# Performance work log

Measured on AMD Instinct MI355X. Metric: run time of the kernel, lower is better.

The kernel has to match this reference:

```python
import jax, jax.numpy as jnp
import numpy as np

N_NODES = 100000
N_EDGES = 3200000
N_FEAT = 128
HIDDEN = 16
N_CLASSES = 10
N_GRAPHS = 64


def gcn_conv(x, W, b, src, dst, num_nodes):
    # PyG GCNConv: h = x W; add self-loops; norm = deg^{-1/2}[src]*deg^{-1/2}[dst]
    h = x @ W  # [N, out]
    deg = jax.ops.segment_sum(jnp.ones(src.shape[0], h.dtype), dst,
                              num_segments=num_nodes) + 1.0  # self-loop
    dinv = jax.lax.rsqrt(deg)
    coef = dinv[src] * dinv[dst]  # [E]
    agg = jax.ops.segment_sum(h[src] * coef[:, None], dst,
                              num_segments=num_nodes)
    # self-loop contribution: norm = dinv[i]^2
    agg = agg + h * (dinv * dinv)[:, None]
    return agg + b


def setup_inputs() -> dict:
    key = jax.random.key(0)
    k1, k2, k3, k4, k5, k6, k7 = jax.random.split(key, 7)
    x = jax.random.normal(k1, (N_NODES, N_FEAT), dtype=jnp.float32)
    edge_index = jax.random.randint(k2, (2, N_EDGES), 0, N_NODES, dtype=jnp.int64)
    batch = jnp.sort(jax.random.randint(k3, (N_NODES,), 0, N_GRAPHS, dtype=jnp.int64))
    W1 = jax.random.normal(k4, (N_FEAT, HIDDEN), dtype=jnp.float32) / np.sqrt(N_FEAT)
    b1 = jnp.zeros((HIDDEN,), jnp.float32)
    W2 = jax.random.normal(k5, (HIDDEN, N_CLASSES), dtype=jnp.float32) / np.sqrt(HIDDEN)
    b2 = jnp.zeros((N_CLASSES,), jnp.float32)
    return {"x": x, "edge_index": edge_index, "batch": batch,
            "W1": W1, "b1": b1, "W2": W2, "b2": b2}


def reference(x, edge_index, batch, W1, b1, W2, b2):
    src, dst = edge_index[0], edge_index[1]
    h = gcn_conv(x, W1, b1, src, dst, N_NODES)
    h = jax.nn.relu(h)
    h = gcn_conv(h, W2, b2, src, dst, N_NODES)  # [N, C]
    # global mean pool per graph
    sums = jax.ops.segment_sum(h, batch, num_segments=N_GRAPHS)
    cnts = jax.ops.segment_sum(jnp.ones(N_NODES, h.dtype), batch,
                               num_segments=N_GRAPHS)
    pooled = sums / jnp.maximum(cnts, 1.0)[:, None]  # [G, C]
    return jax.nn.log_softmax(pooled, axis=1)
```

## Files before the change

kernel.cpp:

```cpp
#include <hip/hip_runtime.h>
#include <hip/hip_fp16.h>

#define N_NODES   100000
#define N_EDGES   3200000
#define N_FEAT    128
#define HIDDEN    16
#define N_CLASSES 10
#define N_GRAPHS  64

#define NBUCK     391
#define CAP       9216
#define BINA_EPB  16384
#define BINA_BLOCKS ((N_EDGES + BINA_EPB - 1) / BINA_EPB)


__global__ __launch_bounds__(512) void k_ginit(int* __restrict__ gcur,
                                               float* __restrict__ pooled) {
    int t = threadIdx.x;
    if (t < NBUCK) gcur[t] = t * CAP;
    pooled[t] = 0.f;
    pooled[t + 512] = 0.f;
}

__global__ __launch_bounds__(1024) void k_binA(const int* __restrict__ src,
                                               const int* __restrict__ dst,
                                               int* __restrict__ gcur,
                                               int* __restrict__ stage) {
    __shared__ int hist[NBUCK];
    __shared__ int curb[NBUCK];
    int tid = threadIdx.x;
    long long base = (long long)blockIdx.x * BINA_EPB;
    for (int t = tid; t < NBUCK; t += 1024) hist[t] = 0;
    __syncthreads();
    int se[16], de[16];
#pragma unroll
    for (int i = 0; i < 16; ++i) {
        long long e = base + i * 1024 + tid;
        if (e < N_EDGES) {
            se[i] = src[e];
            de[i] = dst[e];
            atomicAdd(&hist[de[i] >> 8], 1);
        } else {
            de[i] = -1;
        }
    }
    __syncthreads();
    for (int t = tid; t < NBUCK; t += 1024) {
        int h = hist[t];
        curb[t] = h ? atomicAdd(&gcur[t], h) : 0;
    }
    __syncthreads();
#pragma unroll
    for (int i = 0; i < 16; ++i) {
        if (de[i] >= 0) {
            int b = de[i] >> 8;
            int p = atomicAdd(&curb[b], 1);
            stage[p] = (se[i] << 8) | (de[i] & 255);
        }
    }
}

__global__ __launch_bounds__(512) void k_binB(const int* __restrict__ gcur,
                                              const int* __restrict__ stage,
                                              int2* __restrict__ be,
                                              float* __restrict__ dinv,
                                              int* __restrict__ srcs) {
    __shared__ int hist[256];
    __shared__ int excl[256];
    int b = blockIdx.x, tid = threadIdx.x;
    int cnt   = gcur[b] - b * CAP;
    int sbase = b * CAP;
    if (tid < 256) hist[tid] = 0;
    __syncthreads();
    int nvec = cnt >> 2;
    for (int i = tid; i < nvec; i += 512) {
        int4 v = *(const int4*)&stage[sbase + i * 4];
        atomicAdd(&hist[v.x & 255], 1);
        atomicAdd(&hist[v.y & 255], 1);
        atomicAdd(&hist[v.z & 255], 1);
        atomicAdd(&hist[v.w & 255], 1);
    }
    if (tid < (cnt & 3)) {
        int v = stage[sbase + (nvec << 2) + tid];
        atomicAdd(&hist[v & 255], 1);
    }
    __syncthreads();
    int c = 0, ex = 0;
    if (tid < 256) {
        c = hist[tid];
        excl[tid] = c;
    }
    __syncthreads();
    for (int o = 1; o < 256; o <<= 1) {
        int a = 0;
        if (tid < 256 && tid >= o) a = excl[tid - o];
        __syncthreads();
        if (tid < 256) excl[tid] += a;
        __syncthreads();
    }
    if (tid < 256) {
        ex = excl[tid] - c;
        int node = b * 256 + tid;
        if (node < N_NODES) {
            be[node]   = make_int2(sbase + ex, sbase + ex + c);
            dinv[node] = rsqrtf((float)c + 1.0f);
        }
    }
    __syncthreads();
    if (tid < 256) hist[tid] = ex;
    __syncthreads();
    for (int i = tid; i < nvec; i += 512) {
        int4 v = *(const int4*)&stage[sbase + i * 4];
        int p0 = atomicAdd(&hist[v.x & 255], 1);
        int p1 = atomicAdd(&hist[v.y & 255], 1);
        int p2 = atomicAdd(&hist[v.z & 255], 1);
        int p3 = atomicAdd(&hist[v.w & 255], 1);
        srcs[sbase + p0] = v.x >> 8;
        srcs[sbase + p1] = v.y >> 8;
        srcs[sbase + p2] = v.z >> 8;
        srcs[sbase + p3] = v.w >> 8;
    }
    if (tid < (cnt & 3)) {
        int v = stage[sbase + (nvec << 2) + tid];
        int p = atomicAdd(&hist[v & 255], 1);
        srcs[sbase + p] = v >> 8;
    }
}

__global__ __launch_bounds__(256) void k_gemm1(const float* __restrict__ x,
                                               const float* __restrict__ W1,
                                               const float* __restrict__ dinv,
                                               __half* __restrict__ h1h) {
    __shared__ float w[N_FEAT * HIDDEN];
    __shared__ float xs[16 * N_FEAT];
    __shared__ float ds[16];
    int tid  = threadIdx.x;
    int base = blockIdx.x * 16;
    if (tid < 16) ds[tid] = dinv[base + tid];
    const float4* w4 = (const float4*)W1;
    float4*       wd = (float4*)w;
    wd[tid]       = w4[tid];
    wd[256 + tid] = w4[256 + tid];
    const float4* x4 = (const float4*)(x + (long long)base * N_FEAT);
    float4*       xd = (float4*)xs;
    xd[tid]       = x4[tid];
    xd[256 + tid] = x4[256 + tid];
    __syncthreads();
    int n = tid >> 4, c = tid & 15;
    const float* xr = &xs[n * N_FEAT];
    float acc = 0.f;
#pragma unroll
    for (int k = 0; k < N_FEAT; ++k) acc += xr[k] * w[k * HIDDEN + c];
    h1h[(base + n) * HIDDEN + c] = __float2half(acc * ds[n]);
}

#define NT(p) __builtin_nontemporal_load(p)

#define GATHER_DEF(TBL)                                                       \
    float acc[8];                                                             \
    _Pragma("unroll") for (int q = 0; q < 8; ++q) acc[q] = 0.f;               \
    {                                                                         \
        int ne = end - beg;                                                   \
        int nr = ne >> 3;                                                     \
        int j  = beg + k;                                                     \
        int npair = nr >> 1;                                                  \
        if (npair > 0) {                                                      \
            int sA = NT(&srcs[j]), sB = NT(&srcs[j + 8]);                     \
            for (int p = 1; p < npair; ++p) {                                 \
                int sC = NT(&srcs[j + 16]), sD = NT(&srcs[j + 24]);           \
                GACC(TBL, sA); GACC(TBL, sB);                                 \
                sA = sC; sB = sD; j += 16;                                    \
            }                                                                 \
            GACC(TBL, sA); GACC(TBL, sB); j += 16;                            \
        }                                                                     \
        if (nr & 1) { int sA = NT(&srcs[j]); GACC(TBL, sA); j += 8; }         \
        if (k < (ne & 7)) { int sA = NT(&srcs[j]); GACC(TBL, sA); }           \
    }                                                                         \
    _Pragma("unroll") for (int m = 2; m <= 8; m <<= 1) {                      \
        _Pragma("unroll") for (int q = 0; q < 8; ++q)                         \
            acc[q] += __shfl_xor(acc[q], m, 64);                              \
    }

#define GACC(TBL, S) {                                                        \
    float4 g_ = *(const float4*)(&TBL[(S) * 16 + h * 8]);                     \
    const __half2* hp_ = (const __half2*)&g_;                                 \
    float2 v0_ = __half22float2(hp_[0]);                                      \
    float2 v1_ = __half22float2(hp_[1]);                                      \
    float2 v2_ = __half22float2(hp_[2]);                                      \
    float2 v3_ = __half22float2(hp_[3]);                                      \
    acc[0] += v0_.x; acc[1] += v0_.y; acc[2] += v1_.x; acc[3] += v1_.y;       \
    acc[4] += v2_.x; acc[5] += v2_.y; acc[6] += v3_.x; acc[7] += v3_.y; }

__global__ __launch_bounds__(256) void k_agg1(const int2* __restrict__ be,
                                              const int* __restrict__ srcs,
                                              const float* __restrict__ dinv,
                                              const __half* __restrict__ h1h,
                                              const float* __restrict__ b1,
                                              const float* __restrict__ W2,
                                              __half* __restrict__ h2h) {
    __shared__ float r_s[16][17];
    __shared__ float w2s[HIDDEN * N_CLASSES];
    int tid = threadIdx.x;
    if (tid < HIDDEN * N_CLASSES) w2s[tid] = W2[tid];
    int nl = tid >> 4, l = tid & 15, k = l >> 1, h = l & 1;
    int n  = blockIdx.x * 16 + nl;
    int2 bn = be[n];
    int beg = bn.x, end = bn.y;
    GATHER_DEF(h1h)
    if (l < 2) {
#pragma unroll
        for (int q = 0; q < 8; ++q) r_s[nl][h * 8 + q] = acc[q];
    }
    __syncthreads();
    float dn   = dinv[n];
    float self = __half2float(h1h[n * 16 + l]);
    float val  = fmaxf(dn * (r_s[nl][l] + self) + b1[l], 0.f);
    __syncthreads();
    r_s[nl][l] = val;
    __syncthreads();
    float o = 0.f;
    if (l < N_CLASSES) {
#pragma unroll
        for (int q = 0; q < HIDDEN; ++q) o += r_s[nl][q] * w2s[q * N_CLASSES + l];
        o *= dn;
    }
    h2h[n * 16 + l] = __float2half(o);
}

__global__ __launch_bounds__(256) void k_agg2p(const int2* __restrict__ be,
                                               const int* __restrict__ srcs,
                                               const float* __restrict__ dinv,
                                               const __half* __restrict__ h2h,
                                               const int* __restrict__ batch,
                                               float* __restrict__ pooled) {
    __shared__ float red[16][17];
    int tid = threadIdx.x;
    int nl = tid >> 4, l = tid & 15, k = l >> 1, h = l & 1;
    int nbase = blockIdx.x * 16;
    int n  = nbase + nl;
    int2 bn = be[n];
    int beg = bn.x, end = bn.y;
    GATHER_DEF(h2h)
    if (l < 2) {
#pragma unroll
        for (int q = 0; q < 8; ++q) red[nl][h * 8 + q] = acc[q];
    }
    __syncthreads();
    float self = __half2float(h2h[n * 16 + l]);
    float o = dinv[n] * (red[nl][l] + self);
    __syncthreads();

    int g0  = batch[nbase];
    int g15 = batch[nbase + 15];
    if (g0 == g15) {
        red[nl][l] = o;
        __syncthreads();
#pragma unroll
        for (int s = 8; s > 0; s >>= 1) {
            if (nl < s) red[nl][l] += red[nl + s][l];
            __syncthreads();
        }
        if (tid < N_CLASSES) atomicAdd(&pooled[g0 * 16 + tid], red[0][tid]);
    } else {
        if (l < N_CLASSES) atomicAdd(&pooled[batch[n] * 16 + l], o);
    }
}

__global__ __launch_bounds__(64) void k_final(const float* __restrict__ pooled,
                                              const float* __restrict__ b2,
                                              const int* __restrict__ batch,
                                              float* __restrict__ out) {
    int g = threadIdx.x;
    if (g >= N_GRAPHS) return;
    int lo = 0, hi = N_NODES;
    while (lo < hi) { int m = (lo + hi) >> 1; if (batch[m] < g) lo = m + 1; else hi = m; }
    int start = lo;
    lo = 0; hi = N_NODES;
    while (lo < hi) { int m = (lo + hi) >> 1; if (batch[m] < g + 1) lo = m + 1; else hi = m; }
    int cnt = lo - start;

    float v[N_CLASSES];
    if (cnt > 0) {
        float inv = 1.f / (float)cnt;
#pragma unroll
        for (int j = 0; j < N_CLASSES; ++j) v[j] = pooled[g * 16 + j] * inv + b2[j];
    } else {
#pragma unroll
        for (int j = 0; j < N_CLASSES; ++j) v[j] = 0.f;
    }
    float m = v[0];
#pragma unroll
    for (int j = 1; j < N_CLASSES; ++j) m = fmaxf(m, v[j]);
    float l = 0.f;
#pragma unroll
    for (int j = 0; j < N_CLASSES; ++j) l += expf(v[j] - m);
    l = logf(l);
#pragma unroll
    for (int j = 0; j < N_CLASSES; ++j) out[g * N_CLASSES + j] = v[j] - m - l;
}

extern "C" void kernel_launch(void* const* d_in, const int* in_sizes, int n_in,
                              void* d_out, int out_size, void* d_ws, size_t ws_size,
                              hipStream_t stream) {
    const float* x     = (const float*)d_in[0];
    const int*   edge  = (const int*)d_in[1];
    const int*   batch = (const int*)d_in[2];
    const float* W1    = (const float*)d_in[3];
    const float* b1    = (const float*)d_in[4];
    const float* W2    = (const float*)d_in[5];
    const float* b2    = (const float*)d_in[6];
    float* out = (float*)d_out;
    float* ws  = (float*)d_ws;

    int*    gcur   = (int*)ws;
    float*  pooled = ws + 512;
    float*  dinv   = ws + 1536;
    int2*   be     = (int2*)(ws + 101536);
    int*    srcs   = (int*)(ws + 301536);
    int*    stage  = (int*)(ws + 3904992);
    __half* h1h    = (__half*)(ws + 3904992);
    __half* h2h    = (__half*)(ws + 4704992);

    const int* srcp = edge;
    const int* dstp = edge + N_EDGES;

    k_ginit<<<1, 512, 0, stream>>>(gcur, pooled);
    k_binA<<<BINA_BLOCKS, 1024, 0, stream>>>(srcp, dstp, gcur, stage);
    k_binB<<<NBUCK, 512, 0, stream>>>(gcur, stage, be, dinv, srcs);
    k_gemm1<<<N_NODES / 16, 256, 0, stream>>>(x, W1, dinv, h1h);
    k_agg1<<<N_NODES / 16, 256, 0, stream>>>(be, srcs, dinv, h1h, b1, W2, h2h);
    k_agg2p<<<N_NODES / 16, 256, 0, stream>>>(be, srcs, dinv, h2h, batch, pooled);
    k_final<<<1, 64, 0, stream>>>(pooled, b2, batch, out);
}
```

Measured before the change: 238.6 us.

## Replace atomic bucket binning with per-block fixed slots and vectorize gemm1

The edge binning no longer claims space in each bucket with global atomics. Each binA block now writes its bucket counts into a per-block, per-bucket table, and its edges go into a fixed 128-entry slot for that (block, bucket) pair. binB reads those counts and walks the scattered slots with one wavefront per slot before doing the local counting sort. In gemm1, W1 is transposed into padded shared memory so the dot product uses float4 loads, and the init kernel becomes a memset. The risks are a much larger staging buffer, less contiguous reads in binB, and silent overflow if any (block, bucket) cell exceeds 128 edges.

```diff
diff --git a/kernel.cpp b/kernel.cpp
--- a/kernel.cpp
+++ b/kernel.cpp
@@ -10,21 +10,14 @@
 
 #define NBUCK     391
 #define CAP       9216
+#define SLOT      128
 #define BINA_EPB  16384
 #define BINA_BLOCKS ((N_EDGES + BINA_EPB - 1) / BINA_EPB)
 
 
-__global__ __launch_bounds__(512) void k_ginit(int* __restrict__ gcur,
-                                               float* __restrict__ pooled) {
-    int t = threadIdx.x;
-    if (t < NBUCK) gcur[t] = t * CAP;
-    pooled[t] = 0.f;
-    pooled[t + 512] = 0.f;
-}
-
 __global__ __launch_bounds__(1024) void k_binA(const int* __restrict__ src,
                                                const int* __restrict__ dst,
-                                               int* __restrict__ gcur,
+                                               int* __restrict__ gcnt,
                                                int* __restrict__ stage) {
     __shared__ int hist[NBUCK];
     __shared__ int curb[NBUCK];
@@ -45,9 +38,10 @@
         }
     }
     __syncthreads();
+    int cellbase = blockIdx.x * NBUCK;
     for (int t = tid; t < NBUCK; t += 1024) {
-        int h = hist[t];
-        curb[t] = h ? atomicAdd(&gcur[t], h) : 0;
+        gcnt[cellbase + t] = hist[t];
+        curb[t] = (cellbase + t) * SLOT;
     }
     __syncthreads();
 #pragma unroll
@@ -60,36 +54,30 @@
     }
 }
 
-__global__ __launch_bounds__(512) void k_binB(const int* __restrict__ gcur,
-                                              const int* __restrict__ stage,
-                                              int2* __restrict__ be,
-                                              float* __restrict__ dinv,
-                                              int* __restrict__ srcs) {
+__global__ __launch_bounds__(1024) void k_binB(const int* __restrict__ gcnt,
+                                               const int* __restrict__ stage,
+                                               int2* __restrict__ be,
+                                               float* __restrict__ dinv,
+                                               int* __restrict__ srcs) {
     __shared__ int hist[256];
     __shared__ int excl[256];
+    __shared__ int scnt[BINA_BLOCKS];
     int b = blockIdx.x, tid = threadIdx.x;
-    int cnt   = gcur[b] - b * CAP;
-    int sbase = b * CAP;
     if (tid < 256) hist[tid] = 0;
-    __syncthreads();
-    int nvec = cnt >> 2;
-    for (int i = tid; i < nvec; i += 512) {
-        int4 v = *(const int4*)&stage[sbase + i * 4];
-        atomicAdd(&hist[v.x & 255], 1);
-        atomicAdd(&hist[v.y & 255], 1);
-        atomicAdd(&hist[v.z & 255], 1);
-        atomicAdd(&hist[v.w & 255], 1);
-    }
-    if (tid < (cnt & 3)) {
-        int v = stage[sbase + (nvec << 2) + tid];
-        atomicAdd(&hist[v & 255], 1);
-    }
-    __syncthreads();
-    int c = 0, ex = 0;
-    if (tid < 256) {
-        c = hist[tid];
-        excl[tid] = c;
-    }
+    for (int s = tid; s < BINA_BLOCKS; s += 1024) scnt[s] = gcnt[s * NBUCK + b];
+    __syncthreads();
+    int wid = tid >> 6, lane = tid & 63;
+    for (int s = wid; s < BINA_BLOCKS; s += 16) {
+        int c  = scnt[s];
+        int sb = (s * NBUCK + b) * SLOT;
+        for (int i = lane; i < c; i += 64) {
+            int v = stage[sb + i];
+            atomicAdd(&hist[v & 255], 1);
+        }
+    }
+    __syncthreads();
+    int c = 0;
+    if (tid < 256) { c = hist[tid]; excl[tid] = c; }
     __syncthreads();
     for (int o = 1; o < 256; o <<= 1) {
         int a = 0;
@@ -98,8 +86,9 @@
         if (tid < 256) excl[tid] += a;
         __syncthreads();
     }
+    int sbase = b * CAP;
     if (tid < 256) {
-        ex = excl[tid] - c;
+        int ex = excl[tid] - c;
         int node = b * 256 + tid;
         if (node < N_NODES) {
             be[node]   = make_int2(sbase + ex, sbase + ex + c);
@@ -107,23 +96,16 @@
         }
     }
     __syncthreads();
-    if (tid < 256) hist[tid] = ex;
-    __syncthreads();
-    for (int i = tid; i < nvec; i += 512) {
-        int4 v = *(const int4*)&stage[sbase + i * 4];
-        int p0 = atomicAdd(&hist[v.x & 255], 1);
-        int p1 = atomicAdd(&hist[v.y & 255], 1);
-        int p2 = atomicAdd(&hist[v.z & 255], 1);
-        int p3 = atomicAdd(&hist[v.w & 255], 1);
-        srcs[sbase + p0] = v.x >> 8;
-        srcs[sbase + p1] = v.y >> 8;
-        srcs[sbase + p2] = v.z >> 8;
-        srcs[sbase + p3] = v.w >> 8;
-    }
-    if (tid < (cnt & 3)) {
-        int v = stage[sbase + (nvec << 2) + tid];
-        int p = atomicAdd(&hist[v & 255], 1);
-        srcs[sbase + p] = v >> 8;
+    if (tid < 256) hist[tid] = excl[tid] - c;
+    __syncthreads();
+    for (int s = wid; s < BINA_BLOCKS; s += 16) {
+        int cc = scnt[s];
+        int sb = (s * NBUCK + b) * SLOT;
+        for (int i = lane; i < cc; i += 64) {
+            int v = stage[sb + i];
+            int p = atomicAdd(&hist[v & 255], 1);
+            srcs[sbase + p] = v >> 8;
+        }
     }
 }
 
@@ -131,26 +113,36 @@
                                                const float* __restrict__ W1,
                                                const float* __restrict__ dinv,
                                                __half* __restrict__ h1h) {
-    __shared__ float w[N_FEAT * HIDDEN];
+    __shared__ float wT[16][132];
     __shared__ float xs[16 * N_FEAT];
     __shared__ float ds[16];
     int tid  = threadIdx.x;
     int base = blockIdx.x * 16;
     if (tid < 16) ds[tid] = dinv[base + tid];
     const float4* w4 = (const float4*)W1;
-    float4*       wd = (float4*)w;
-    wd[tid]       = w4[tid];
-    wd[256 + tid] = w4[256 + tid];
+    float4 wa = w4[tid], wb = w4[256 + tid];
+    {
+        int r = tid >> 2, cb = (tid & 3) * 4;
+        wT[cb + 0][r] = wa.x; wT[cb + 1][r] = wa.y;
+        wT[cb + 2][r] = wa.z; wT[cb + 3][r] = wa.w;
+        int r2 = r + 64;
+        wT[cb + 0][r2] = wb.x; wT[cb + 1][r2] = wb.y;
+        wT[cb + 2][r2] = wb.z; wT[cb + 3][r2] = wb.w;
+    }
     const float4* x4 = (const float4*)(x + (long long)base * N_FEAT);
     float4*       xd = (float4*)xs;
     xd[tid]       = x4[tid];
     xd[256 + tid] = x4[256 + tid];
     __syncthreads();
     int n = tid >> 4, c = tid & 15;
-    const float* xr = &xs[n * N_FEAT];
+    const float4* xv = (const float4*)&xs[n * N_FEAT];
+    const float4* wv = (const float4*)&wT[c][0];
     float acc = 0.f;
 #pragma unroll
-    for (int k = 0; k < N_FEAT; ++k) acc += xr[k] * w[k * HIDDEN + c];
+    for (int k4 = 0; k4 < 32; ++k4) {
+        float4 a = xv[k4], w = wv[k4];
+        acc += a.x * w.x + a.y * w.y + a.z * w.z + a.w * w.w;
+    }
     h1h[(base + n) * HIDDEN + c] = __float2half(acc * ds[n]);
 }
 
@@ -312,21 +304,21 @@
     float* out = (float*)d_out;
     float* ws  = (float*)d_ws;
 
-    int*    gcur   = (int*)ws;
-    float*  pooled = ws + 512;
-    float*  dinv   = ws + 1536;
-    int2*   be     = (int2*)(ws + 101536);
-    int*    srcs   = (int*)(ws + 301536);
-    int*    stage  = (int*)(ws + 3904992);
-    __half* h1h    = (__half*)(ws + 3904992);
-    __half* h2h    = (__half*)(ws + 4704992);
+    float*  pooled = ws;
+    float*  dinv   = ws + 1024;
+    int2*   be     = (int2*)(ws + 101024);
+    int*    gcnt   = (int*)(ws + 301024);
+    int*    srcs   = (int*)(ws + 377660);
+    int*    stage  = (int*)(ws + 3981120);
+    __half* h1h    = (__half*)(ws + 3981120);
+    __half* h2h    = (__half*)(ws + 4781120);
 
     const int* srcp = edge;
     const int* dstp = edge + N_EDGES;
 
-    k_ginit<<<1, 512, 0, stream>>>(gcur, pooled);
-    k_binA<<<BINA_BLOCKS, 1024, 0, stream>>>(srcp, dstp, gcur, stage);
-    k_binB<<<NBUCK, 512, 0, stream>>>(gcur, stage, be, dinv, srcs);
+    hipMemsetAsync(pooled, 0, 1024 * sizeof(float), stream);
+    k_binA<<<BINA_BLOCKS, 1024, 0, stream>>>(srcp, dstp, gcnt, stage);
+    k_binB<<<NBUCK, 1024, 0, stream>>>(gcnt, stage, be, dinv, srcs);
     k_gemm1<<<N_NODES / 16, 256, 0, stream>>>(x, W1, dinv, h1h);
     k_agg1<<<N_NODES / 16, 256, 0, stream>>>(be, srcs, dinv, h1h, b1, W2, h2h);
     k_agg2p<<<N_NODES / 16, 256, 0, stream>>>(be, srcs, dinv, h2h, batch, pooled);
```

New measurement: 238.8 us. Within noise of the previous version (+0.1%).
